# Optimization experiments

Hardware: AMD Instinct MI355X
Metric: run time of the kernel (lower is better)

## Reference

```python
import jax, jax.numpy as jnp
import numpy as np

HIDDEN = 1024
FFN = 2048
N_EXPERTS = 8
TOP_K = 2


def setup_inputs() -> dict:
    key = jax.random.key(0)
    k_x, k_g, k1, k2, k3 = jax.random.split(key, 5)
    hidden_states = jax.random.normal(k_x, (4, 4096, HIDDEN), dtype=jnp.float32)
    gate_w = jax.random.normal(k_g, (N_EXPERTS, HIDDEN), dtype=jnp.float32) * 0.02
    # nn.Linear convention: weight is [out_features, in_features]
    w1 = jax.random.normal(k1, (N_EXPERTS, FFN, HIDDEN), dtype=jnp.float32) * 0.02
    w2 = jax.random.normal(k2, (N_EXPERTS, HIDDEN, FFN), dtype=jnp.float32) * 0.02
    w3 = jax.random.normal(k3, (N_EXPERTS, FFN, HIDDEN), dtype=jnp.float32) * 0.02
    return {"hidden_states": hidden_states, "gate_w": gate_w, "w1": w1, "w2": w2, "w3": w3}


def reference(hidden_states, gate_w, w1, w2, w3):
    B, S, H = hidden_states.shape
    E = gate_w.shape[0]
    x = hidden_states.reshape(-1, H)  # [T, H]
    T = x.shape[0]

    # Router: softmax in fp32, top-2, renormalize (matches torch reference)
    router_logits = jnp.einsum("th,eh->te", x, gate_w)
    probs = jax.nn.softmax(router_logits.astype(jnp.float32), axis=-1)
    top_w, top_i = jax.lax.top_k(probs, TOP_K)  # [T, 2]
    top_w = top_w / jnp.sum(top_w, axis=-1, keepdims=True)
    top_w = top_w.astype(x.dtype)

    # Dense combine weights [T, E]: zero for unselected experts.
    combine = jnp.zeros((T, E), dtype=x.dtype)
    combine = combine.at[jnp.arange(T)[:, None], top_i].set(top_w)

    # Per-expert SwiGLU; loop over small fixed expert count, accumulate.
    out = jnp.zeros_like(x)
    for e in range(E):
        h = jax.nn.silu(x @ w1[e].T) * (x @ w3[e].T)  # [T, FFN]
        out = out + combine[:, e:e + 1] * (h @ w2[e].T)
    return out.reshape(B, S, H)
```

## Files before the change

kernel.cpp:

```cpp
#include <hip/hip_runtime.h>
#include <cstdint>

#define H 1024
#define F 2048
#define E_N 8
#define BM 256
#define BK 64

typedef __attribute__((ext_vector_type(8))) short short8v;
typedef __attribute__((ext_vector_type(4))) float float4v;
typedef unsigned short u16;

__device__ __forceinline__ u16 f2bf(float f) {
    uint32_t u = __float_as_uint(f);
    u += 0x7FFFu + ((u >> 16) & 1u);
    return (u16)(u >> 16);
}
__device__ __forceinline__ float bf2f(u16 b) {
    return __uint_as_float(((uint32_t)b) << 16);
}

__device__ __forceinline__ void gload16(const void* g, void* l) {
    __builtin_amdgcn_global_load_lds((const __attribute__((address_space(1))) uint32_t*)g,
                                     (__attribute__((address_space(3))) uint32_t*)l, 16, 0, 0);
}

__device__ __forceinline__ void barx() {
    asm volatile("" ::: "memory");
    __builtin_amdgcn_s_barrier();
    asm volatile("" ::: "memory");
}

__device__ __forceinline__ void decode_swz(int bid, int nTiles, int ngy, int gyc,
                                           int& tile, int& gy) {
    int nblk = nTiles * ngy;
    int q = nblk >> 3, r = nblk & 7;
    int xcd = bid & 7, pos = bid >> 3;
    int cid = (xcd < r ? xcd * (q + 1) : r * (q + 1) + (xcd - r) * q) + pos;
    int per = nTiles * gyc;
    int chunk = cid / per, rem = cid - chunk * per;
    tile = rem / gyc;
    gy = chunk * gyc + (rem - (rem / gyc) * gyc);
}

__global__ __launch_bounds__(256) void cvt_kernel(const float* __restrict__ src,
                                                  u16* __restrict__ dst, int n) {
    int i = (blockIdx.x * 256 + threadIdx.x) * 4;
    int stride = gridDim.x * 256 * 4;
    for (; i < n; i += stride) {
        float4 v = *(const float4*)(src + i);
        ushort4 o;
        o.x = f2bf(v.x); o.y = f2bf(v.y); o.z = f2bf(v.z); o.w = f2bf(v.w);
        *(ushort4*)(dst + i) = o;
    }
}

__global__ __launch_bounds__(256) void router_kernel(const float* __restrict__ x,
                                                     const float* __restrict__ gw,
                                                     int* __restrict__ topi,
                                                     float* __restrict__ topw, int T) {
    int wave = threadIdx.x >> 6, lane = threadIdx.x & 63;
    int t = blockIdx.x * 4 + wave;
    if (t >= T) return;
    const float4* xr = (const float4*)(x + (size_t)t * H);
    float4 xv[4];
#pragma unroll
    for (int i = 0; i < 4; i++) xv[i] = xr[i * 64 + lane];
    float acc[E_N];
#pragma unroll
    for (int e = 0; e < E_N; e++) {
        const float4* gr = (const float4*)(gw + e * H);
        float s = 0.f;
#pragma unroll
        for (int i = 0; i < 4; i++) {
            float4 g = gr[i * 64 + lane];
            s += xv[i].x * g.x + xv[i].y * g.y + xv[i].z * g.z + xv[i].w * g.w;
        }
        acc[e] = s;
    }
#pragma unroll
    for (int e = 0; e < E_N; e++) {
#pragma unroll
        for (int off = 32; off; off >>= 1) acc[e] += __shfl_xor(acc[e], off, 64);
    }
    if (lane == 0) {
        int i0 = 0;
#pragma unroll
        for (int e = 1; e < E_N; e++) if (acc[e] > acc[i0]) i0 = e;
        int i1 = -1;
#pragma unroll
        for (int e = 0; e < E_N; e++) {
            if (e == i0) continue;
            if (i1 < 0 || acc[e] > acc[i1]) i1 = e;
        }
        float e1 = __expf(acc[i1] - acc[i0]);
        float w0 = 1.f / (1.f + e1);
        float w1v = e1 / (1.f + e1);
        topi[t * 2] = i0; topi[t * 2 + 1] = i1;
        topw[t * 2] = w0; topw[t * 2 + 1] = w1v;
    }
}

__global__ __launch_bounds__(256) void hist_kernel(const int* __restrict__ topi,
                                                   int* __restrict__ counts, int n) {
    __shared__ int hc[E_N];
    if (threadIdx.x < E_N) hc[threadIdx.x] = 0;
    __syncthreads();
    for (int i = blockIdx.x * 256 + threadIdx.x; i < n; i += gridDim.x * 256)
        atomicAdd(&hc[topi[i]], 1);
    __syncthreads();
    if (threadIdx.x < E_N) atomicAdd(&counts[threadIdx.x], hc[threadIdx.x]);
}

__global__ void scan_kernel(const int* __restrict__ counts, int* __restrict__ offsets,
                            int* __restrict__ cursors, int* __restrict__ tileOff) {
    if (threadIdx.x == 0 && blockIdx.x == 0) {
        int o = 0, to = 0;
        for (int e = 0; e < E_N; e++) {
            offsets[e] = o; cursors[e] = o; tileOff[e] = to;
            o += counts[e];
            to += (counts[e] + BM - 1) / BM;
        }
        offsets[E_N] = o; tileOff[E_N] = to;
    }
}

__global__ __launch_bounds__(1024) void scatter_kernel(const int* __restrict__ topi,
                                                       const float* __restrict__ topw,
                                                       int* __restrict__ cursors,
                                                       int* __restrict__ perm_tok,
                                                       float* __restrict__ perm_gate,
                                                       int* __restrict__ inv, int n) {
    __shared__ int hc[E_N];
    __shared__ int base[E_N];
    int tid = threadIdx.x;
    if (tid < E_N) hc[tid] = 0;
    __syncthreads();
    int i = blockIdx.x * 1024 + tid;
    int e = 0, lrank = 0;
    bool ok = (i < n);
    if (ok) {
        e = topi[i];
        lrank = atomicAdd(&hc[e], 1);
    }
    __syncthreads();
    if (tid < E_N) base[tid] = atomicAdd(&cursors[tid], hc[tid]);
    __syncthreads();
    if (ok) {
        int pos = base[e] + lrank;
        perm_tok[pos] = i >> 1;
        perm_gate[pos] = topw[i];
        inv[i] = pos;
    }
}

__global__ __launch_bounds__(512) void stage1_kernel(
    const u16* __restrict__ xg, const u16* __restrict__ w1b, const u16* __restrict__ w3b,
    const int* __restrict__ perm_tok, const float* __restrict__ perm_gate,
    const int* __restrict__ offsets, const int* __restrict__ tileOff,
    u16* __restrict__ h, int cstart, int tpcThis) {
    __shared__ u16 lA[2 * BM * BK];
    __shared__ u16 lB1[2 * 128 * BK];
    __shared__ u16 lB3[2 * 128 * BK];
    __shared__ int ptokS[BM];
    __shared__ float pgateS[BM];

    int tileL, nbIdx;
    decode_swz(blockIdx.x, tpcThis, F / 128, 4, tileL, nbIdx);
    int tile = cstart + tileL;
    if (tile >= tileOff[E_N]) return;
    int e = 0;
    while (e < E_N - 1 && tile >= tileOff[e + 1]) e++;
    int rbase = offsets[e] + (tile - tileOff[e]) * BM;
    int segEnd = offsets[e + 1];
    int e0 = 0;
    while (e0 < E_N - 1 && cstart >= tileOff[e0 + 1]) e0++;
    int chunkBase = offsets[e0] + (cstart - tileOff[e0]) * BM;

    int tid = threadIdx.x;
    if (tid < BM) {
        int p = rbase + tid; if (p > segEnd - 1) p = segEnd - 1;
        ptokS[tid] = perm_tok[p];
        pgateS[tid] = perm_gate[p];
    }
    __syncthreads();

    int lane = tid & 63, wid = tid >> 6;
    int wr = wid >> 2, wc = wid & 3;
    int lrow = lane & 15, kgrp = lane >> 4;
    int lr = lane >> 3, csw = ((lane & 7) ^ lr) << 3;
    int nb = nbIdx * 128;
    const u16* w1p = w1b + (size_t)e * F * H + (size_t)nb * H;
    const u16* w3p = w3b + (size_t)e * F * H + (size_t)nb * H;

    const u16* pA[4];
#pragma unroll
    for (int j = 0; j < 4; j++) pA[j] = xg + (size_t)ptokS[(j * 8 + wid) * 8 + lr] * H + csw;
    const u16 *pB1[2], *pB3[2];
#pragma unroll
    for (int j = 0; j < 2; j++) {
        int rr = (j * 8 + wid) * 8 + lr;
        pB1[j] = w1p + (size_t)rr * H + csw;
        pB3[j] = w3p + (size_t)rr * H + csw;
    }

    int swe0 = (kgrp ^ (lrow & 7)) << 3;
    int swe1 = ((4 + kgrp) ^ (lrow & 7)) << 3;
    int eA0 = (wr * 128 + lrow) * BK + swe0;
    int eA1 = (wr * 128 + lrow) * BK + swe1;
    int eB0 = (wc * 32 + lrow) * BK + swe0;
    int eB1 = (wc * 32 + lrow) * BK + swe1;

#define STA(CC, j)  gload16(pA[j],  &lA[(CC) * 16384 + ((j) * 8 + wid) * 8 * BK])
#define STB1(CC, j) gload16(pB1[j], &lB1[(CC) * 8192 + ((j) * 8 + wid) * 8 * BK])
#define STB3(CC, j) gload16(pB3[j], &lB3[(CC) * 8192 + ((j) * 8 + wid) * 8 * BK])

    float4v acc1[8][2], acc3[8][2];
#pragma unroll
    for (int a = 0; a < 8; a++)
#pragma unroll
        for (int b = 0; b < 2; b++) { acc1[a][b] = (float4v)(0.f); acc3[a][b] = (float4v)(0.f); }

    STB1(0, 0); STB1(0, 1);
    STB3(0, 0); STB3(0, 1);
    STA(0, 0); STA(0, 2); STA(0, 1); STA(0, 3);
#pragma unroll
    for (int j = 0; j < 4; j++) pA[j] += BK;
    pB1[0] += BK; pB1[1] += BK; pB3[0] += BK; pB3[1] += BK;
    asm volatile("s_waitcnt vmcnt(2)" ::: "memory");
    barx();

#define S1_DSA(CC, p) \
    short8v aF[2][2]; \
    _Pragma("unroll") \
    for (int pm = 0; pm < 2; pm++) { \
        aF[pm][0] = *(const short8v*)&lA[eA0 + (CC) * 16384 + (2 * (p) + pm) * 1024]; \
        aF[pm][1] = *(const short8v*)&lA[eA1 + (CC) * 16384 + (2 * (p) + pm) * 1024]; \
    }
#define S1_MM(p) \
    __builtin_amdgcn_s_setprio(1); \
    _Pragma("unroll") \
    for (int pm = 0; pm < 2; pm++) \
    _Pragma("unroll") \
    for (int n = 0; n < 2; n++) \
    _Pragma("unroll") \
    for (int kk = 0; kk < 2; kk++) { \
        acc1[2 * (p) + pm][n] = __builtin_amdgcn_mfma_f32_16x16x32_bf16(aF[pm][kk], b1F[n][kk], acc1[2 * (p) + pm][n], 0, 0, 0); \
        acc3[2 * (p) + pm][n] = __builtin_amdgcn_mfma_f32_16x16x32_bf16(aF[pm][kk], b3F[n][kk], acc3[2 * (p) + pm][n], 0, 0, 0); \
    } \
    __builtin_amdgcn_s_setprio(0);

#define S1_KT(CC, LAST) { \
    short8v b1F[2][2], b3F[2][2]; \
    _Pragma("unroll") \
    for (int n = 0; n < 2; n++) { \
        b1F[n][0] = *(const short8v*)&lB1[eB0 + (CC) * 8192 + n * 1024]; \
        b1F[n][1] = *(const short8v*)&lB1[eB1 + (CC) * 8192 + n * 1024]; \
        b3F[n][0] = *(const short8v*)&lB3[eB0 + (CC) * 8192 + n * 1024]; \
        b3F[n][1] = *(const short8v*)&lB3[eB1 + (CC) * 8192 + n * 1024]; \
    } \
    { S1_DSA(CC, 0) \
      if (!(LAST)) { STB1((CC) ^ 1, 0); STB1((CC) ^ 1, 1); } \
      barx(); S1_MM(0) barx(); } \
    { S1_DSA(CC, 1) \
      if (!(LAST)) { STB3((CC) ^ 1, 0); STB3((CC) ^ 1, 1); } \
      barx(); S1_MM(1) \
      if (!(LAST)) { asm volatile("s_waitcnt vmcnt(4)" ::: "memory"); } \
      else         { asm volatile("s_waitcnt vmcnt(0)" ::: "memory"); } \
      barx(); } \
    { S1_DSA(CC, 2) \
      if (!(LAST)) { STA((CC) ^ 1, 0); STA((CC) ^ 1, 2); } \
      barx(); S1_MM(2) barx(); } \
    { S1_DSA(CC, 3) \
      if (!(LAST)) { STA((CC) ^ 1, 1); STA((CC) ^ 1, 3); } \
      barx(); S1_MM(3) \
      asm volatile("s_waitcnt vmcnt(2)" ::: "memory"); \
      barx(); } \
    _Pragma("unroll") \
    for (int j = 0; j < 4; j++) pA[j] += BK; \
    pB1[0] += BK; pB1[1] += BK; pB3[0] += BK; pB3[1] += BK; \
}

    for (int tt = 0; tt < (H / BK) - 2; tt += 2) {
        S1_KT(0, false)
        S1_KT(1, false)
    }
    S1_KT(0, false)
    S1_KT(1, true)
#undef S1_DSA
#undef S1_MM
#undef S1_KT
#undef STA
#undef STB1
#undef STB3

    int rif = (lane >> 4) * 4;
#pragma unroll
    for (int m = 0; m < 8; m++) {
#pragma unroll
        for (int reg = 0; reg < 4; reg++) {
            int rowIdx = wr * 128 + m * 16 + rif + reg;
            int p = rbase + rowIdx;
            if (p < segEnd) {
                float g = pgateS[rowIdx];
#pragma unroll
                for (int n = 0; n < 2; n++) {
                    float a1 = acc1[m][n][reg], a3 = acc3[m][n][reg];
                    float sv = a1 / (1.f + __expf(-a1));
                    float hv = sv * a3 * g;
                    int ncol = nb + wc * 32 + n * 16 + (lane & 15);
                    h[(size_t)(p - chunkBase) * F + ncol] = f2bf(hv);
                }
            }
        }
    }
}

template<int NREP>
__global__ __launch_bounds__(512) void stage2_kernel(
    const u16* __restrict__ h, const u16* __restrict__ w2b,
    const int* __restrict__ offsets, const int* __restrict__ tileOff,
    u16* __restrict__ y, int cstart, int tpcThis) {
    constexpr int BN = NREP * 64;
    constexpr int BSTRIDE = BN * BK;
    __shared__ u16 lA[2 * BM * BK];
    __shared__ u16 lB[2 * BSTRIDE];

    int tileL, nbIdx;
    decode_swz(blockIdx.x, tpcThis, H / BN, 4, tileL, nbIdx);
    int tile = cstart + tileL;
    if (tile >= tileOff[E_N]) return;
    int e = 0;
    while (e < E_N - 1 && tile >= tileOff[e + 1]) e++;
    int rbase = offsets[e] + (tile - tileOff[e]) * BM;
    int segEnd = offsets[e + 1];
    int e0 = 0;
    while (e0 < E_N - 1 && cstart >= tileOff[e0 + 1]) e0++;
    int chunkBase = offsets[e0] + (cstart - tileOff[e0]) * BM;

    int tid = threadIdx.x;
    int lane = tid & 63, wid = tid >> 6;
    int wr = wid >> 2, wc = wid & 3;
    int lrow = lane & 15, kgrp = lane >> 4;
    int lr = lane >> 3, csw = ((lane & 7) ^ lr) << 3;
    int nb = nbIdx * BN;
    const u16* w2p = w2b + (size_t)e * H * F + (size_t)nb * F;

    const u16* pA[4];
#pragma unroll
    for (int j = 0; j < 4; j++) {
        int rb = (j * 8 + wid) * 8;
        int p = rbase + rb + lr; if (p > segEnd - 1) p = segEnd - 1;
        pA[j] = h + (size_t)(p - chunkBase) * F + csw;
    }
    const u16* pB[NREP];
#pragma unroll
    for (int j = 0; j < NREP; j++) pB[j] = w2p + (size_t)((j * 8 + wid) * 8 + lr) * F + csw;

    int swe0 = (kgrp ^ (lrow & 7)) << 3;
    int swe1 = ((4 + kgrp) ^ (lrow & 7)) << 3;
    int eA0 = (wr * 128 + lrow) * BK + swe0;
    int eA1 = (wr * 128 + lrow) * BK + swe1;
    int eB0 = (wc * (NREP * 16) + lrow) * BK + swe0;
    int eB1 = (wc * (NREP * 16) + lrow) * BK + swe1;

#define STA2(CC, j) gload16(pA[j], &lA[(CC) * 16384 + ((j) * 8 + wid) * 8 * BK])
#define STB2(CC, j) gload16(pB[j], &lB[(CC) * BSTRIDE + ((j) * 8 + wid) * 8 * BK])

    float4v acc[8][NREP];
#pragma unroll
    for (int a = 0; a < 8; a++)
#pragma unroll
        for (int b = 0; b < NREP; b++) acc[a][b] = (float4v)(0.f);

#pragma unroll
    for (int j = 0; j < NREP; j++) STB2(0, j);
    STA2(0, 0); STA2(0, 2); STA2(0, 1); STA2(0, 3);
#pragma unroll
    for (int j = 0; j < 4; j++) pA[j] += BK;
#pragma unroll
    for (int j = 0; j < NREP; j++) pB[j] += BK;
    asm volatile("s_waitcnt vmcnt(2)" ::: "memory");
    barx();

#define S2_DSA(CC, p) \
    short8v aF[2][2]; \
    _Pragma("unroll") \
    for (int pm = 0; pm < 2; pm++) { \
        aF[pm][0] = *(const short8v*)&lA[eA0 + (CC) * 16384 + (2 * (p) + pm) * 1024]; \
        aF[pm][1] = *(const short8v*)&lA[eA1 + (CC) * 16384 + (2 * (p) + pm) * 1024]; \
    }
#define S2_MM(p) \
    __builtin_amdgcn_s_setprio(1); \
    _Pragma("unroll") \
    for (int pm = 0; pm < 2; pm++) \
    _Pragma("unroll") \
    for (int n = 0; n < NREP; n++) \
    _Pragma("unroll") \
    for (int kk = 0; kk < 2; kk++) \
        acc[2 * (p) + pm][n] = __builtin_amdgcn_mfma_f32_16x16x32_bf16(aF[pm][kk], bF[n][kk], acc[2 * (p) + pm][n], 0, 0, 0); \
    __builtin_amdgcn_s_setprio(0);

#define S2_KT(CC, LAST) { \
    short8v bF[NREP][2]; \
    _Pragma("unroll") \
    for (int n = 0; n < NREP; n++) { \
        bF[n][0] = *(const short8v*)&lB[eB0 + (CC) * BSTRIDE + n * 1024]; \
        bF[n][1] = *(const short8v*)&lB[eB1 + (CC) * BSTRIDE + n * 1024]; \
    } \
    { S2_DSA(CC, 0) \
      if (!(LAST)) { STB2((CC) ^ 1, 0); if (NREP == 4) STB2((CC) ^ 1, 1); } \
      barx(); S2_MM(0) barx(); } \
    { S2_DSA(CC, 1) \
      if (!(LAST)) { if (NREP == 4) { STB2((CC) ^ 1, 2); STB2((CC) ^ 1, 3); } else STB2((CC) ^ 1, 1); } \
      barx(); S2_MM(1) \
      if (!(LAST)) { \
          if (NREP == 4) { asm volatile("s_waitcnt vmcnt(4)" ::: "memory"); } \
          else           { asm volatile("s_waitcnt vmcnt(2)" ::: "memory"); } \
      } else { asm volatile("s_waitcnt vmcnt(0)" ::: "memory"); } \
      barx(); } \
    { S2_DSA(CC, 2) \
      if (!(LAST)) { STA2((CC) ^ 1, 0); STA2((CC) ^ 1, 2); } \
      barx(); S2_MM(2) barx(); } \
    { S2_DSA(CC, 3) \
      if (!(LAST)) { STA2((CC) ^ 1, 1); STA2((CC) ^ 1, 3); } \
      barx(); S2_MM(3) \
      asm volatile("s_waitcnt vmcnt(2)" ::: "memory"); \
      barx(); } \
    _Pragma("unroll") \
    for (int j = 0; j < 4; j++) pA[j] += BK; \
    _Pragma("unroll") \
    for (int j = 0; j < NREP; j++) pB[j] += BK; \
}

    for (int tt = 0; tt < (F / BK) - 2; tt += 2) {
        S2_KT(0, false)
        S2_KT(1, false)
    }
    S2_KT(0, false)
    S2_KT(1, true)
#undef S2_DSA
#undef S2_MM
#undef S2_KT
#undef STA2
#undef STB2

    int rif = (lane >> 4) * 4;
#pragma unroll
    for (int m = 0; m < 8; m++) {
#pragma unroll
        for (int reg = 0; reg < 4; reg++) {
            int rowIdx = wr * 128 + m * 16 + rif + reg;
            int p = rbase + rowIdx;
            if (p < segEnd) {
#pragma unroll
                for (int n = 0; n < NREP; n++) {
                    int col = nb + wc * (BN / 4) + n * 16 + (lane & 15);
                    y[(size_t)p * H + col] = f2bf(acc[m][n][reg]);
                }
            }
        }
    }
}

__global__ __launch_bounds__(256) void combine_kernel(const u16* __restrict__ y,
                                                      const int* __restrict__ inv,
                                                      float* __restrict__ out) {
    int t = blockIdx.x, c = threadIdx.x;
    int s0 = inv[t * 2], s1 = inv[t * 2 + 1];
    ushort4 a = *(const ushort4*)(y + (size_t)s0 * H + c * 4);
    ushort4 b = *(const ushort4*)(y + (size_t)s1 * H + c * 4);
    float4 o;
    o.x = bf2f(a.x) + bf2f(b.x);
    o.y = bf2f(a.y) + bf2f(b.y);
    o.z = bf2f(a.z) + bf2f(b.z);
    o.w = bf2f(a.w) + bf2f(b.w);
    *(float4*)(out + (size_t)t * H + c * 4) = o;
}

extern "C" void kernel_launch(void* const* d_in, const int* in_sizes, int n_in,
                              void* d_out, int out_size, void* d_ws, size_t ws_size,
                              hipStream_t stream) {
    (void)n_in; (void)out_size;
    const float* x  = (const float*)d_in[0];
    const float* gw = (const float*)d_in[1];
    const float* w1 = (const float*)d_in[2];
    const float* w2 = (const float*)d_in[3];
    const float* w3 = (const float*)d_in[4];
    float* out = (float*)d_out;
    int T = in_sizes[0] / H;
    int P = T * 2;

    char* ws = (char*)d_ws;
    size_t off = 0;
    auto alloc = [&](size_t b) { size_t c = off; off = (off + b + 255) & ~(size_t)255; return c; };
    size_t misc_o  = alloc(256);
    int* counts  = (int*)(ws + misc_o);
    int* offsets = (int*)(ws + misc_o + 64);
    int* cursors = (int*)(ws + misc_o + 128);
    int* tileOff = (int*)(ws + misc_o + 192);
    size_t topi_o  = alloc((size_t)T * 2 * 4);
    size_t topw_o  = alloc((size_t)T * 2 * 4);
    size_t ptok_o  = alloc((size_t)P * 4);
    size_t pgate_o = alloc((size_t)P * 4);
    size_t inv_o   = alloc((size_t)T * 2 * 4);
    size_t w1b_o = alloc((size_t)E_N * F * H * 2);
    size_t w3b_o = alloc((size_t)E_N * F * H * 2);
    size_t w2b_o = alloc((size_t)E_N * H * F * 2);
    size_t xg_o  = alloc((size_t)T * H * 2);
    size_t y_o   = alloc((size_t)P * H * 2);

    int maxTiles = P / BM + E_N;
    size_t perTile = (size_t)BM * F * 2;
    size_t avail = (ws_size > off + 256) ? (ws_size - off - 256) : 0;
    int tpc = (int)(avail / perTile);
    if (tpc > maxTiles) tpc = maxTiles;
    if (tpc < 4) tpc = 4;
    size_t h_o = alloc((size_t)tpc * perTile);

    hipMemsetAsync(ws + misc_o, 0, 256, stream);

    int nW = E_N * F * H;
    cvt_kernel<<<4096, 256, 0, stream>>>(w1, (u16*)(ws + w1b_o), nW);
    cvt_kernel<<<4096, 256, 0, stream>>>(w3, (u16*)(ws + w3b_o), nW);
    cvt_kernel<<<4096, 256, 0, stream>>>(w2, (u16*)(ws + w2b_o), nW);
    cvt_kernel<<<4096, 256, 0, stream>>>(x,  (u16*)(ws + xg_o),  T * H);

    router_kernel<<<T / 4, 256, 0, stream>>>(x, gw, (int*)(ws + topi_o), (float*)(ws + topw_o), T);
    hist_kernel<<<32, 256, 0, stream>>>((int*)(ws + topi_o), counts, P);
    scan_kernel<<<1, 64, 0, stream>>>(counts, offsets, cursors, tileOff);
    scatter_kernel<<<(P + 1023) / 1024, 1024, 0, stream>>>(
        (int*)(ws + topi_o), (float*)(ws + topw_o), cursors,
        (int*)(ws + ptok_o), (float*)(ws + pgate_o), (int*)(ws + inv_o), P);

    for (int cstart = 0; cstart < maxTiles; cstart += tpc) {
        int tpcThis = maxTiles - cstart; if (tpcThis > tpc) tpcThis = tpc;
        stage1_kernel<<<tpcThis * (F / 128), 512, 0, stream>>>(
            (u16*)(ws + xg_o), (u16*)(ws + w1b_o), (u16*)(ws + w3b_o),
            (int*)(ws + ptok_o), (float*)(ws + pgate_o), offsets, tileOff,
            (u16*)(ws + h_o), cstart, tpcThis);
        if (tpcThis >= 54)
            stage2_kernel<4><<<tpcThis * (H / 256), 512, 0, stream>>>(
                (u16*)(ws + h_o), (u16*)(ws + w2b_o), offsets, tileOff,
                (u16*)(ws + y_o), cstart, tpcThis);
        else
            stage2_kernel<2><<<tpcThis * (H / 128), 512, 0, stream>>>(
                (u16*)(ws + h_o), (u16*)(ws + w2b_o), offsets, tileOff,
                (u16*)(ws + y_o), cstart, tpcThis);
    }
    combine_kernel<<<T, 256, 0, stream>>>((u16*)(ws + y_o), (int*)(ws + inv_o), out);
}
```

Before: 640.0 us.

## Merge weight conversions, fuse x cast into router, rebalance GEMM prefetch

The three weight fp32-to-bf16 conversions now run as one launch over a contiguous buffer, and the activation cast is folded into the router kernel, which already reads x. This removes three launches and one extra pass over x. In both GEMM stages the A-tile prefetch loads are spread across the four sub-steps instead of being bunched in the last two, and the vmcnt waits are adjusted to match. This gives more overlap of global loads with MFMA work, but if the outstanding-load counts are wrong it risks ordering hazards.

```diff
diff --git a/kernel.cpp b/kernel.cpp
--- a/kernel.cpp
+++ b/kernel.cpp
@@ -6,6 +6,7 @@
 #define E_N 8
 #define BM 256
 #define BK 64
+#define NW (E_N * F * H)
 
 typedef __attribute__((ext_vector_type(8))) short short8v;
 typedef __attribute__((ext_vector_type(4))) float float4v;
@@ -43,12 +44,17 @@
     gy = chunk * gyc + (rem - (rem / gyc) * gyc);
 }
 
-__global__ __launch_bounds__(256) void cvt_kernel(const float* __restrict__ src,
-                                                  u16* __restrict__ dst, int n) {
+__global__ __launch_bounds__(256) void cvt3_kernel(const float* __restrict__ s0,
+                                                   const float* __restrict__ s1,
+                                                   const float* __restrict__ s2,
+                                                   u16* __restrict__ dst) {
     int i = (blockIdx.x * 256 + threadIdx.x) * 4;
     int stride = gridDim.x * 256 * 4;
-    for (; i < n; i += stride) {
-        float4 v = *(const float4*)(src + i);
+    for (; i < 3 * NW; i += stride) {
+        int seg = i / NW;
+        int off = i - seg * NW;
+        const float* s = (seg == 0) ? s0 : ((seg == 1) ? s1 : s2);
+        float4 v = *(const float4*)(s + off);
         ushort4 o;
         o.x = f2bf(v.x); o.y = f2bf(v.y); o.z = f2bf(v.z); o.w = f2bf(v.w);
         *(ushort4*)(dst + i) = o;
@@ -58,7 +64,8 @@
 __global__ __launch_bounds__(256) void router_kernel(const float* __restrict__ x,
                                                      const float* __restrict__ gw,
                                                      int* __restrict__ topi,
-                                                     float* __restrict__ topw, int T) {
+                                                     float* __restrict__ topw,
+                                                     u16* __restrict__ xg, int T) {
     int wave = threadIdx.x >> 6, lane = threadIdx.x & 63;
     int t = blockIdx.x * 4 + wave;
     if (t >= T) return;
@@ -66,6 +73,13 @@
     float4 xv[4];
 #pragma unroll
     for (int i = 0; i < 4; i++) xv[i] = xr[i * 64 + lane];
+#pragma unroll
+    for (int i = 0; i < 4; i++) {
+        ushort4 o;
+        o.x = f2bf(xv[i].x); o.y = f2bf(xv[i].y);
+        o.z = f2bf(xv[i].z); o.w = f2bf(xv[i].w);
+        *(ushort4*)(xg + (size_t)t * H + (i * 64 + lane) * 4) = o;
+    }
     float acc[E_N];
 #pragma unroll
     for (int e = 0; e < E_N; e++) {
@@ -260,19 +274,19 @@
         b3F[n][1] = *(const short8v*)&lB3[eB1 + (CC) * 8192 + n * 1024]; \
     } \
     { S1_DSA(CC, 0) \
-      if (!(LAST)) { STB1((CC) ^ 1, 0); STB1((CC) ^ 1, 1); } \
+      if (!(LAST)) { STB1((CC) ^ 1, 0); STB1((CC) ^ 1, 1); STA((CC) ^ 1, 0); } \
       barx(); S1_MM(0) barx(); } \
     { S1_DSA(CC, 1) \
-      if (!(LAST)) { STB3((CC) ^ 1, 0); STB3((CC) ^ 1, 1); } \
+      if (!(LAST)) { STB3((CC) ^ 1, 0); STB3((CC) ^ 1, 1); STA((CC) ^ 1, 2); } \
       barx(); S1_MM(1) \
-      if (!(LAST)) { asm volatile("s_waitcnt vmcnt(4)" ::: "memory"); } \
+      if (!(LAST)) { asm volatile("s_waitcnt vmcnt(6)" ::: "memory"); } \
       else         { asm volatile("s_waitcnt vmcnt(0)" ::: "memory"); } \
       barx(); } \
     { S1_DSA(CC, 2) \
-      if (!(LAST)) { STA((CC) ^ 1, 0); STA((CC) ^ 1, 2); } \
+      if (!(LAST)) { STA((CC) ^ 1, 1); } \
       barx(); S1_MM(2) barx(); } \
     { S1_DSA(CC, 3) \
-      if (!(LAST)) { STA((CC) ^ 1, 1); STA((CC) ^ 1, 3); } \
+      if (!(LAST)) { STA((CC) ^ 1, 3); } \
       barx(); S1_MM(3) \
       asm volatile("s_waitcnt vmcnt(2)" ::: "memory"); \
       barx(); } \
@@ -409,21 +423,22 @@
         bF[n][1] = *(const short8v*)&lB[eB1 + (CC) * BSTRIDE + n * 1024]; \
     } \
     { S2_DSA(CC, 0) \
-      if (!(LAST)) { STB2((CC) ^ 1, 0); if (NREP == 4) STB2((CC) ^ 1, 1); } \
+      if (!(LAST)) { STB2((CC) ^ 1, 0); if (NREP == 4) STB2((CC) ^ 1, 1); STA2((CC) ^ 1, 0); } \
       barx(); S2_MM(0) barx(); } \
     { S2_DSA(CC, 1) \
-      if (!(LAST)) { if (NREP == 4) { STB2((CC) ^ 1, 2); STB2((CC) ^ 1, 3); } else STB2((CC) ^ 1, 1); } \
+      if (!(LAST)) { if (NREP == 4) { STB2((CC) ^ 1, 2); STB2((CC) ^ 1, 3); } else STB2((CC) ^ 1, 1); \
+                     STA2((CC) ^ 1, 2); } \
       barx(); S2_MM(1) \
       if (!(LAST)) { \
-          if (NREP == 4) { asm volatile("s_waitcnt vmcnt(4)" ::: "memory"); } \
-          else           { asm volatile("s_waitcnt vmcnt(2)" ::: "memory"); } \
+          if (NREP == 4) { asm volatile("s_waitcnt vmcnt(6)" ::: "memory"); } \
+          else           { asm volatile("s_waitcnt vmcnt(4)" ::: "memory"); } \
       } else { asm volatile("s_waitcnt vmcnt(0)" ::: "memory"); } \
       barx(); } \
     { S2_DSA(CC, 2) \
-      if (!(LAST)) { STA2((CC) ^ 1, 0); STA2((CC) ^ 1, 2); } \
+      if (!(LAST)) { STA2((CC) ^ 1, 1); } \
       barx(); S2_MM(2) barx(); } \
     { S2_DSA(CC, 3) \
-      if (!(LAST)) { STA2((CC) ^ 1, 1); STA2((CC) ^ 1, 3); } \
+      if (!(LAST)) { STA2((CC) ^ 1, 3); } \
       barx(); S2_MM(3) \
       asm volatile("s_waitcnt vmcnt(2)" ::: "memory"); \
       barx(); } \
@@ -504,11 +519,12 @@
     size_t ptok_o  = alloc((size_t)P * 4);
     size_t pgate_o = alloc((size_t)P * 4);
     size_t inv_o   = alloc((size_t)T * 2 * 4);
-    size_t w1b_o = alloc((size_t)E_N * F * H * 2);
-    size_t w3b_o = alloc((size_t)E_N * F * H * 2);
-    size_t w2b_o = alloc((size_t)E_N * H * F * 2);
+    size_t wb_o  = alloc((size_t)3 * NW * 2);
     size_t xg_o  = alloc((size_t)T * H * 2);
     size_t y_o   = alloc((size_t)P * H * 2);
+    u16* w1b = (u16*)(ws + wb_o);
+    u16* w3b = w1b + NW;
+    u16* w2b = w1b + 2 * (size_t)NW;
 
     int maxTiles = P / BM + E_N;
     size_t perTile = (size_t)BM * F * 2;
@@ -520,13 +536,9 @@
 
     hipMemsetAsync(ws + misc_o, 0, 256, stream);
 
-    int nW = E_N * F * H;
-    cvt_kernel<<<4096, 256, 0, stream>>>(w1, (u16*)(ws + w1b_o), nW);
-    cvt_kernel<<<4096, 256, 0, stream>>>(w3, (u16*)(ws + w3b_o), nW);
-    cvt_kernel<<<4096, 256, 0, stream>>>(w2, (u16*)(ws + w2b_o), nW);
-    cvt_kernel<<<4096, 256, 0, stream>>>(x,  (u16*)(ws + xg_o),  T * H);
-
-    router_kernel<<<T / 4, 256, 0, stream>>>(x, gw, (int*)(ws + topi_o), (float*)(ws + topw_o), T);
+    cvt3_kernel<<<8192, 256, 0, stream>>>(w1, w3, w2, w1b);
+    router_kernel<<<T / 4, 256, 0, stream>>>(x, gw, (int*)(ws + topi_o), (float*)(ws + topw_o),
+                                             (u16*)(ws + xg_o), T);
     hist_kernel<<<32, 256, 0, stream>>>((int*)(ws + topi_o), counts, P);
     scan_kernel<<<1, 64, 0, stream>>>(counts, offsets, cursors, tileOff);
     scatter_kernel<<<(P + 1023) / 1024, 1024, 0, stream>>>(
@@ -536,16 +548,16 @@
     for (int cstart = 0; cstart < maxTiles; cstart += tpc) {
         int tpcThis = maxTiles - cstart; if (tpcThis > tpc) tpcThis = tpc;
         stage1_kernel<<<tpcThis * (F / 128), 512, 0, stream>>>(
-            (u16*)(ws + xg_o), (u16*)(ws + w1b_o), (u16*)(ws + w3b_o),
+            (u16*)(ws + xg_o), w1b, w3b,
             (int*)(ws + ptok_o), (float*)(ws + pgate_o), offsets, tileOff,
             (u16*)(ws + h_o), cstart, tpcThis);
         if (tpcThis >= 54)
             stage2_kernel<4><<<tpcThis * (H / 256), 512, 0, stream>>>(
-                (u16*)(ws + h_o), (u16*)(ws + w2b_o), offsets, tileOff,
+                (u16*)(ws + h_o), w2b, offsets, tileOff,
                 (u16*)(ws + y_o), cstart, tpcThis);
         else
             stage2_kernel<2><<<tpcThis * (H / 128), 512, 0, stream>>>(
-                (u16*)(ws + h_o), (u16*)(ws + w2b_o), offsets, tileOff,
+                (u16*)(ws + h_o), w2b, offsets, tileOff,
                 (u16*)(ws + y_o), cstart, tpcThis);
     }
     combine_kernel<<<T, 256, 0, stream>>>((u16*)(ws + y_o), (int*)(ws + inv_o), out);
```

After: 640.3 us. About the same (+0.0%).
